# Optimization experiments

Hardware: AMD Instinct MI355X
Metric: run time of the kernel (lower is better)

The kernel has to match this reference:

```python
import jax, jax.numpy as jnp
import numpy as np

PC_RANGE = [-51.2, -51.2, -5.0, 51.2, 51.2, 3.0]
VOXEL = [0.1, 0.1, 0.2]
OSF = 8
NUM_PRIOR = 100
C = 256
BN_EPS = 1e-5
LN_EPS = 1e-5


def _conv(x, w, pad):
    # x: [B,C,H,W], w: [O,I,kh,kw]
    return jax.lax.conv_general_dilated(
        x, w, window_strides=(1, 1), padding=[(pad, pad), (pad, pad)],
        dimension_numbers=('NCHW', 'OIHW', 'NCHW'))


def _bn(x, g, b, m, v):
    scale = (g / jnp.sqrt(v + BN_EPS))[None, :, None, None]
    return (x - m[None, :, None, None]) * scale + b[None, :, None, None]


def setup_inputs() -> dict:
    key = jax.random.key(0)
    ks = jax.random.split(key, 24)
    s3 = 1.0 / np.sqrt(C * 9)
    s1 = 1.0 / np.sqrt(C)
    inp = {
        'bev_feat': jax.random.normal(ks[0], (4, C, 128, 128), jnp.float32),
        'template_anchor': jax.random.normal(ks[1], (4, 900, 11), jnp.float32),
        # shared_conv: 3x3 conv (no bias) + BN(eval) + ReLU
        'shared_w': jax.random.normal(ks[2], (C, C, 3, 3), jnp.float32) * s3,
        'bn1_g': jax.random.normal(ks[3], (C,), jnp.float32) * 0.1 + 1.0,
        'bn1_b': jax.random.normal(ks[4], (C,), jnp.float32) * 0.1,
        'bn1_m': jax.random.normal(ks[5], (C,), jnp.float32) * 0.1,
        'bn1_v': jax.random.uniform(ks[6], (C,), jnp.float32) + 0.5,
        # objectness: 3x3 conv (no bias) + BN + ReLU + 1x1 conv (bias=-2)
        'obj_w1': jax.random.normal(ks[7], (C, C, 3, 3), jnp.float32) * s3,
        'bn2_g': jax.random.normal(ks[8], (C,), jnp.float32) * 0.1 + 1.0,
        'bn2_b': jax.random.normal(ks[9], (C,), jnp.float32) * 0.1,
        'bn2_m': jax.random.normal(ks[10], (C,), jnp.float32) * 0.1,
        'bn2_v': jax.random.uniform(ks[11], (C,), jnp.float32) + 0.5,
        'obj_w2': jax.random.normal(ks[12], (1, C, 1, 1), jnp.float32) * s1,
        'obj_b2': jnp.full((1,), -2.0, jnp.float32),
        # feat_proj: Linear + LN + ReLU + Linear
        'fp_w1': jax.random.normal(ks[13], (C, C), jnp.float32) * s1,
        'fp_b1': jax.random.normal(ks[14], (C,), jnp.float32) * 0.01,
        'ln_g': jnp.ones((C,), jnp.float32),
        'ln_b': jnp.zeros((C,), jnp.float32),
        'fp_w2': jax.random.normal(ks[15], (C, C), jnp.float32) * s1,
        'fp_b2': jax.random.normal(ks[16], (C,), jnp.float32) * 0.01,
        # geometry heads (1x1 convs, bias init 0)
        'z_w': jax.random.normal(ks[17], (1, C, 1, 1), jnp.float32) * s1,
        'z_b': jnp.zeros((1,), jnp.float32),
        'dim_w': jax.random.normal(ks[18], (3, C, 1, 1), jnp.float32) * s1,
        'dim_b': jnp.zeros((3,), jnp.float32),
        'yaw_w': jax.random.normal(ks[19], (2, C, 1, 1), jnp.float32) * s1,
        'yaw_b': jnp.zeros((2,), jnp.float32),
        'vel_w': jax.random.normal(ks[20], (2, C, 1, 1), jnp.float32) * s1,
        'vel_b': jnp.zeros((2,), jnp.float32),
    }
    return inp


def _forward(bev_feat, template_anchor, shared_w, bn1_g, bn1_b, bn1_m, bn1_v,
             obj_w1, bn2_g, bn2_b, bn2_m, bn2_v, obj_w2, obj_b2,
             fp_w1, fp_b1, ln_g, ln_b, fp_w2, fp_b2,
             z_w, z_b, dim_w, dim_b, yaw_w, yaw_b, vel_w, vel_b):
    B, Cc, H, W = bev_feat.shape
    # shared_conv
    feat = jax.nn.relu(_bn(_conv(bev_feat, shared_w, 1), bn1_g, bn1_b, bn1_m, bn1_v))
    # objectness heatmap
    h = jax.nn.relu(_bn(_conv(feat, obj_w1, 1), bn2_g, bn2_b, bn2_m, bn2_v))
    heatmap = jax.nn.sigmoid(_conv(h, obj_w2, 0) + obj_b2[None, :, None, None])
    score = heatmap.reshape(B, H * W)
    K = min(NUM_PRIOR, H * W, template_anchor.shape[1])
    topk_score, topk_inds = jax.lax.top_k(score, K)  # [B,K]
    ys = topk_inds // W
    xs = topk_inds % W
    # gather BEV features at topk locations: [B,K,C]
    feat_flat = feat.reshape(B, Cc, H * W).transpose(0, 2, 1)
    gathered = jnp.take_along_axis(feat_flat, topk_inds[:, :, None], axis=1)
    # feat_proj: Linear + LN + ReLU + Linear
    x = gathered @ fp_w1.T + fp_b1
    mu = jnp.mean(x, axis=-1, keepdims=True)
    var = jnp.mean((x - mu) ** 2, axis=-1, keepdims=True)
    x = (x - mu) / jnp.sqrt(var + LN_EPS) * ln_g + ln_b
    x = jax.nn.relu(x)
    prior_feature = x @ fp_w2.T + fp_b2
    prior_feature = prior_feature * (1.0 + topk_score[:, :, None])
    # geometry heads (1x1 convs == linear on gathered features)
    z_pred = gathered @ z_w[:, :, 0, 0].T + z_b      # [B,K,1]
    dim_pred = gathered @ dim_w[:, :, 0, 0].T + dim_b  # [B,K,3]
    yaw_pred = gathered @ yaw_w[:, :, 0, 0].T + yaw_b  # [B,K,2]
    vel_pred = gathered @ vel_w[:, :, 0, 0].T + vel_b  # [B,K,2]
    # anchor update
    pa = template_anchor[:, :K, :]
    x_metric = (xs.astype(pa.dtype) + 0.5) * (VOXEL[0] * OSF) + PC_RANGE[0]
    y_metric = (ys.astype(pa.dtype) + 0.5) * (VOXEL[1] * OSF) + PC_RANGE[1]
    z_new = pa[..., 2] + 0.5 * z_pred[..., 0]
    dims_new = pa[..., 3:6] + 0.2 * jnp.clip(dim_pred, -1.0, 1.0)
    yaw = jnp.tanh(yaw_pred)
    nrm = jnp.maximum(jnp.sqrt(jnp.sum(yaw * yaw, axis=-1, keepdims=True)), 1e-6)
    yaw_new = 0.7 * pa[..., 6:8] + 0.3 * (yaw / nrm)
    vel_new = pa[..., 8:10] + 0.2 * jnp.clip(vel_pred, -2.0, 2.0)
    prior_anchor = jnp.concatenate([
        x_metric[..., None], y_metric[..., None], z_new[..., None],
        dims_new, yaw_new, vel_new, pa[..., 10:]], axis=-1)
    return prior_feature, prior_anchor, topk_score


def reference(bev_feat, template_anchor, shared_w, bn1_g, bn1_b, bn1_m, bn1_v,
              obj_w1, bn2_g, bn2_b, bn2_m, bn2_v, obj_w2, obj_b2,
              fp_w1, fp_b1, ln_g, ln_b, fp_w2, fp_b2,
              z_w, z_b, dim_w, dim_b, yaw_w, yaw_b, vel_w, vel_b):
    return _forward(bev_feat, template_anchor, shared_w, bn1_g, bn1_b, bn1_m, bn1_v,
                    obj_w1, bn2_g, bn2_b, bn2_m, bn2_v, obj_w2, obj_b2,
                    fp_w1, fp_b1, ln_g, ln_b, fp_w2, fp_b2,
                    z_w, z_b, dim_w, dim_b, yaw_w, yaw_b, vel_w, vel_b)
```

## Files before the change

kernel.cpp:

```cpp
#include <hip/hip_runtime.h>
#include <math.h>


typedef __attribute__((ext_vector_type(8))) short bf16x8;
typedef __attribute__((ext_vector_type(4))) float f32x4;

#define HW 16384
#define WPITCH 130
#define CCAP 192
#define PSTR 28
#define WSO_XN    0ULL
#define WSO_FEATB 34078720ULL
#define WSO_WP1   68157440ULL
#define WSO_WP2   69337088ULL
#define WSO_BNP   70516736ULL
#define WSO_LOG   70521856ULL
#define WSO_CAND  70784000ULL
#define WSO_CNT   70787072ULL
#define WSO_EXL   70787136ULL
#define WSO_TIDX  70790208ULL
#define WSO_TLOG  70791808ULL
#define WSO_W1N   70793408ULL
#define WSO_W2N   73152704ULL
#define WSO_A1P   WSO_XN
#define WSO_ACC2  28311552ULL

__device__ __forceinline__ float bf2f(short s) {
  return __uint_as_float(((unsigned)(unsigned short)s) << 16);
}
__device__ __forceinline__ short f2bf(float f) {
  unsigned u = __float_as_uint(f);
  u += 0x7fffu + ((u >> 16) & 1u);
  return (short)(u >> 16);
}
__device__ __forceinline__ void gll16(const void* g, void* l) {
  __builtin_amdgcn_global_load_lds(
      (const __attribute__((address_space(1))) void*)g,
      (__attribute__((address_space(3))) void*)l, 16, 0, 0);
}

__global__ void wprep2(const float* __restrict__ s1, const float* __restrict__ s2,
                       short* __restrict__ wp1, short* __restrict__ wp2,
                       float* __restrict__ wn1, float* __restrict__ wn2) {
  int bx = blockIdx.x;
  const float* src;
  short* wp;
  float* wn;
  if (bx >= 2304) {
    src = s2; wp = wp2; wn = wn2; bx -= 2304;
  } else {
    src = s1; wp = wp1; wn = wn1;
  }
  int i = bx * 256 + threadIdx.x;
  float v = src[i];
  int k = i % 9;
  int r = i / 9;
  int ci = r & 255;
  int co = r >> 8;
  wp[(k * 256 + co) * 256 + ci] = f2bf(v);
  wn[(ci * 9 + k) * 256 + co] = v;
}

__global__ void smallprep(const float* g1, const float* b1, const float* m1,
                          const float* v1, const float* g2, const float* b2,
                          const float* m2, const float* v2, const float* w2,
                          const float* ob2, float* __restrict__ bnp,
                          short* __restrict__ xn, short* __restrict__ featb,
                          float* __restrict__ logits) {
  const int blk = blockIdx.x, t = threadIdx.x;
  if (blk < 1024) {
    int i = blk * 256 + t;
    int c = i & 255;
    int r = i >> 8;
    int nh = r >> 1;
    int side = r & 1;
    size_t off = ((size_t)nh * WPITCH + (side ? 129 : 0)) * 256 + c;
    xn[off] = 0;
    featb[off] = 0;
  } else if (blk < 1280) {
    logits[(blk - 1024) * 256 + t] = ob2[0];
  } else {
    float s1 = g1[t] / sqrtf(v1[t] + 1e-5f);
    bnp[t] = s1;
    bnp[256 + t] = b1[t] - m1[t] * s1;
    float s2 = g2[t] / sqrtf(v2[t] + 1e-5f);
    bnp[512 + t] = s2;
    bnp[768 + t] = b2[t] - m2[t] * s2;
    bnp[1024 + t] = w2[t];
  }
}

__global__ __launch_bounds__(256) void nchw2nhwc(const float* __restrict__ in,
                                                 short* __restrict__ out) {
  __shared__ short tl[64 * 66];
  int n = blockIdx.z, c0 = blockIdx.y * 64, s0 = blockIdx.x * 64;
  int sl = threadIdx.x & 63, cl = threadIdx.x >> 6;
  for (int p = 0; p < 16; ++p) {
    int c = cl + p * 4;
    tl[c * 66 + sl] = f2bf(in[(((size_t)(n * 256 + c0 + c)) << 14) + s0 + sl]);
  }
  __syncthreads();
  int co = threadIdx.x & 63, so = threadIdx.x >> 6;
  for (int p = 0; p < 16; ++p) {
    int S = s0 + so + p * 4;
    int h = S >> 7, w = S & 127;
    out[(((size_t)(n * 128 + h)) * WPITCH + w + 1) * 256 + c0 + co] =
        tl[co * 66 + (so + p * 4)];
  }
}

template <int OUT_LOGITS>
__global__ __launch_bounds__(256, 2) void conv3x3(const short* __restrict__ inp,
                                                  const short* __restrict__ wp,
                                                  const float* __restrict__ scale,
                                                  const float* __restrict__ shift,
                                                  const float* __restrict__ w2f,
                                                  short* __restrict__ outb,
                                                  float* __restrict__ logits) {
  __shared__ short a_sm[2][132 * 32];
  __shared__ short b_sm[3][128 * 32];
  const int t = threadIdx.x;
  const int wv = t >> 6, lane = t & 63;
  const int l15 = lane & 15, quad = lane >> 4;
  const int tile = blockIdx.x;
  const int img = tile >> 6;
  const int h0 = (tile & 63) << 1;
  const int nblk = blockIdx.y;
  const int m0 = (wv & 1) << 6;
  const int n0 = (wv >> 1) << 6;

  f32x4 acc[2][4][4];
#pragma unroll
  for (int r = 0; r < 2; ++r)
#pragma unroll
    for (int i = 0; i < 4; ++i)
#pragma unroll
      for (int j = 0; j < 4; ++j) {
        acc[r][i][j][0] = 0.f; acc[r][i][j][1] = 0.f;
        acc[r][i][j][2] = 0.f; acc[r][i][j][3] = 0.f;
      }

  for (int dhi = 0; dhi < 3; ++dhi) {
    const int hy0 = h0 + dhi - 1;
    const int hy1 = hy0 + 1;
    const bool v0 = (hy0 >= 0) && (hy0 <= 127);
    const bool v1 = (hy1 <= 127);
    const size_t arow0 = ((size_t)(img * 128 + hy0)) * WPITCH;
    const size_t arow1 = ((size_t)(img * 128 + hy1)) * WPITCH;
    const short* wbase = wp + ((size_t)(dhi * 3 * 256 + nblk * 128)) * 256;

    for (int c0 = 0; c0 < 256; c0 += 32) {
      __syncthreads();
      if (v0) {
#pragma unroll
        for (int j = 0; j < 2; ++j) {
          const int seg = (j << 6) + (t >> 2);
          const int cc = t & 3;
          gll16(inp + (arow0 + seg) * 256 + c0 + cc * 8,
                a_sm[0] + ((size_t)((j << 8) + t)) * 8);
        }
      }
      if (v1) {
#pragma unroll
        for (int j = 0; j < 2; ++j) {
          const int seg = (j << 6) + (t >> 2);
          const int cc = t & 3;
          gll16(inp + (arow1 + seg) * 256 + c0 + cc * 8,
                a_sm[1] + ((size_t)((j << 8) + t)) * 8);
        }
      }
      if (t < 64) {
        const int row = t >> 5;
        const bool vr = row ? v1 : v0;
        if (vr) {
          const size_t ar = row ? arow1 : arow0;
          const int rem = t & 31;
          const int r2 = rem >> 4, dw = rem & 15;
          const int* gsrc = (const int*)(inp + (ar + 128 + r2) * 256 + c0) + dw;
          ((int*)a_sm[row])[(128 + r2) * 16 + dw] = *gsrc;
        }
      }
#pragma unroll
      for (int dwi = 0; dwi < 3; ++dwi) {
        const short* wtap = wbase + (size_t)dwi * 65536;
#pragma unroll
        for (int j = 0; j < 2; ++j) {
          const int nrow = (j << 6) + (t >> 2);
          const int cc = t & 3;
          gll16(wtap + (size_t)nrow * 256 + c0 + cc * 8,
                b_sm[dwi] + ((size_t)((j << 8) + t)) * 8);
        }
      }
      __syncthreads();

#pragma unroll
      for (int dwi = 0; dwi < 3; ++dwi) {
        bf16x8 bfr[4];
#pragma unroll
        for (int i = 0; i < 4; ++i)
          bfr[i] = *(const bf16x8*)(b_sm[dwi] + (n0 + i * 16 + l15) * 32 + quad * 8);
        if (v0) {
          bf16x8 af[4];
#pragma unroll
          for (int i = 0; i < 4; ++i)
            af[i] = *(const bf16x8*)(a_sm[0] + (dwi + m0 + i * 16 + l15) * 32 + quad * 8);
#pragma unroll
          for (int i = 0; i < 4; ++i)
#pragma unroll
            for (int j = 0; j < 4; ++j)
              acc[0][i][j] = __builtin_amdgcn_mfma_f32_16x16x32_bf16(
                  af[i], bfr[j], acc[0][i][j], 0, 0, 0);
        }
        if (v1) {
          bf16x8 af[4];
#pragma unroll
          for (int i = 0; i < 4; ++i)
            af[i] = *(const bf16x8*)(a_sm[1] + (dwi + m0 + i * 16 + l15) * 32 + quad * 8);
#pragma unroll
          for (int i = 0; i < 4; ++i)
#pragma unroll
            for (int j = 0; j < 4; ++j)
              acc[1][i][j] = __builtin_amdgcn_mfma_f32_16x16x32_bf16(
                  af[i], bfr[j], acc[1][i][j], 0, 0, 0);
        }
      }
    }
  }

  float sc[4], sh[4], wf[4];
#pragma unroll
  for (int j = 0; j < 4; ++j) {
    const int co = nblk * 128 + n0 + j * 16 + l15;
    sc[j] = scale[co];
    sh[j] = shift[co];
    if (OUT_LOGITS) wf[j] = w2f[co];
  }
#pragma unroll
  for (int r = 0; r < 2; ++r) {
    if (OUT_LOGITS) {
      float* lrow = logits + ((size_t)img << 14) + ((h0 + r) << 7);
#pragma unroll
      for (int i = 0; i < 4; ++i) {
#pragma unroll
        for (int rg = 0; rg < 4; ++rg) {
          float part = 0.f;
#pragma unroll
          for (int j = 0; j < 4; ++j) {
            float v = fmaxf(acc[r][i][j][rg] * sc[j] + sh[j], 0.f);
            part += v * wf[j];
          }
          part += __shfl_xor(part, 1);
          part += __shfl_xor(part, 2);
          part += __shfl_xor(part, 4);
          part += __shfl_xor(part, 8);
          if (l15 == 0)
            atomicAdd(&lrow[m0 + i * 16 + quad * 4 + rg], part);
        }
      }
    } else {
      const size_t obase = ((size_t)(img * 128 + h0 + r)) * WPITCH + 1;
#pragma unroll
      for (int i = 0; i < 4; ++i) {
#pragma unroll
        for (int j = 0; j < 4; ++j) {
          const int co = nblk * 128 + n0 + j * 16 + l15;
#pragma unroll
          for (int rg = 0; rg < 4; ++rg) {
            const int m = m0 + i * 16 + quad * 4 + rg;
            float v = fmaxf(acc[r][i][j][rg] * sc[j] + sh[j], 0.f);
            outb[(obase + m) * 256 + co] = f2bf(v);
          }
        }
      }
    }
  }
}

__global__ __launch_bounds__(1024) void topk_radix(const float* __restrict__ logits,
                                                   int* __restrict__ cand,
                                                   int* __restrict__ cnt_out) {
  __shared__ int hist[2048];
  __shared__ int wsum[16];
  __shared__ unsigned sel_bin;
  __shared__ int sel_above;
  __shared__ int cntr;
  const int b = blockIdx.x, t = threadIdx.x;
  const int lane = t & 63, wid = t >> 6;
  const float* L = logits + (size_t)b * HW;
  const int base = t * 16;
  unsigned kv[16];
#pragma unroll
  for (int i = 0; i < 4; ++i) {
    float4 v = *(const float4*)(L + base + i * 4);
    float f4[4] = {v.x, v.y, v.z, v.w};
#pragma unroll
    for (int j = 0; j < 4; ++j) {
      unsigned u = __float_as_uint(f4[j]);
      kv[i * 4 + j] = u ^ (((unsigned)((int)u >> 31)) | 0x80000000u);
    }
  }
  unsigned prefix = 0, pmask = 0;
  int need = 128;
  const int shifts[3] = {21, 10, 0};
  const int nbs[3] = {2048, 2048, 1024};

  for (int lev = 0; lev < 3; ++lev) {
    const int shift = shifts[lev];
    const int nb = nbs[lev];
    hist[t] = 0;
    hist[t + 1024] = 0;
    __syncthreads();
#pragma unroll
    for (int i = 0; i < 16; ++i)
      if ((kv[i] & pmask) == prefix)
        atomicAdd(&hist[(kv[i] >> shift) & (nb - 1)], 1);
    __syncthreads();
    const int cs = nb >> 10;
    const int bin_hi = nb - 1 - t * cs;
    const int c_hi = hist[bin_hi];
    const int c_lo = (cs == 2) ? hist[bin_hi - 1] : 0;
    const int s = c_hi + c_lo;
    int inc = s;
    for (int off = 1; off < 64; off <<= 1) {
      int nbr = __shfl_up(inc, off);
      if (lane >= off) inc += nbr;
    }
    if (lane == 63) wsum[wid] = inc;
    __syncthreads();
    if (wid == 0) {
      int wv = (lane < 16) ? wsum[lane] : 0;
      for (int off = 1; off < 16; off <<= 1) {
        int nbr = __shfl_up(wv, off);
        if (lane >= off) wv += nbr;
      }
      if (lane < 16) wsum[lane] = wv;
    }
    __syncthreads();
    const int excl = inc - s + (wid ? wsum[wid - 1] : 0);
    if (excl < need && need <= excl + s) {
      if (need <= excl + c_hi) {
        sel_bin = (unsigned)bin_hi;
        sel_above = excl;
      } else {
        sel_bin = (unsigned)(bin_hi - 1);
        sel_above = excl + c_hi;
      }
    }
    __syncthreads();
    prefix |= sel_bin << shift;
    pmask |= ((unsigned)(nb - 1)) << shift;
    need -= sel_above;
    __syncthreads();
  }
  if (t == 0) cntr = 0;
  __syncthreads();
#pragma unroll
  for (int i = 0; i < 16; ++i) {
    if (kv[i] >= prefix) {
      int p = atomicAdd(&cntr, 1);
      if (p < CCAP) cand[b * CCAP + p] = base + i;
    }
  }
  __syncthreads();
  if (t == 0) cnt_out[b] = (cntr < CCAP) ? cntr : CCAP;
}

__device__ __forceinline__ void wload4(const float* __restrict__ wr,
                                       float w[4][9]) {
#pragma unroll
  for (int k = 0; k < 9; ++k)
#pragma unroll
    for (int h = 0; h < 4; ++h)
      w[h][k] = wr[k * 256 + (h << 6)];
}

__device__ __forceinline__ void conv_step(const float* __restrict__ pc,
                                          const float w[4][9], float a[4][9]) {
  float xp[28];
  const float4* pr = (const float4*)pc;
#pragma unroll
  for (int q = 0; q < 7; ++q) {
    float4 v = pr[q];
    xp[q * 4 + 0] = v.x; xp[q * 4 + 1] = v.y;
    xp[q * 4 + 2] = v.z; xp[q * 4 + 3] = v.w;
  }
#pragma unroll
  for (int py = 0; py < 3; ++py)
#pragma unroll
    for (int px = 0; px < 3; ++px)
#pragma unroll
      for (int ky = 0; ky < 3; ++ky)
#pragma unroll
        for (int kx = 0; kx < 3; ++kx) {
          const float xv = xp[(py + ky) * 5 + px + kx];
          const int pp = py * 3 + px, kk = ky * 3 + kx;
          a[0][pp] += w[0][kk] * xv;
          a[1][pp] += w[1][kk] * xv;
          a[2][pp] += w[2][kk] * xv;
          a[3][pp] += w[3][kk] * xv;
        }
}

__global__ __launch_bounds__(256, 2) void rescore_a(
    const float* __restrict__ bev, const float* __restrict__ w1n,
    const int* __restrict__ cand, const int* __restrict__ cnt,
    float* __restrict__ a1part) {
  const int bx = blockIdx.x, b = blockIdx.y, z = blockIdx.z;
  const int t = threadIdx.x;
  const int n = cnt[b];
  const int c0 = bx * 4;
  if (c0 >= n) return;
  const int nc = (n - c0 < 4) ? (n - c0) : 4;
  const int ci0 = z << 6;
  __shared__ float patch[4 * 64 * PSTR];

  {
    const int TE = nc * 1600;
    int sg[4];
#pragma unroll
    for (int g = 0; g < 4; ++g) {
      int cc = c0 + g;
      sg[g] = cand[b * CCAP + ((cc < n) ? cc : (n - 1))];
    }
#pragma unroll
    for (int k = 0; k < 25; ++k) {
      int e = t + (k << 8);
      if (e < TE) {
        int g = (e >= 3200) ? ((e >= 4800) ? 3 : 2) : ((e >= 1600) ? 1 : 0);
        int rem = e - g * 1600;
        int ci = rem / 25;
        int rj = rem - ci * 25;
        int r = rj / 5;
        int j = rj - r * 5;
        int s = sg[g];
        int hy = (s >> 7) - 2 + r, wx = (s & 127) - 2 + j;
        float v = 0.f;
        if (hy >= 0 && hy < 128 && wx >= 0 && wx < 128)
          v = bev[(((size_t)(b * 256 + ci0 + ci)) << 14) + (hy << 7) + wx];
        patch[(g * 64 + ci) * PSTR + rj] = v;
      } else {
        int g2z = (e >= 3200) ? ((e >= 4800) ? 3 : 2) : 1;
        int rem = e - g2z * 1600;
        int ci = rem / 25;
        int rj = rem - ci * 25;
        patch[(g2z * 64 + ci) * PSTR + rj] = 0.f;
      }
    }
  }
  __syncthreads();

  const int col = t & 63;
  const int g = t >> 6;
  float a[4][9];
#pragma unroll
  for (int h = 0; h < 4; ++h)
#pragma unroll
    for (int p = 0; p < 9; ++p) a[h][p] = 0.f;

  const float* pbase = patch + (g << 6) * PSTR;
  const float* wbase = w1n + (size_t)ci0 * 2304 + col;

  float wA[4][9], wB[4][9];
  wload4(wbase, wA);
  for (int ci = 0; ci < 64; ci += 2) {
    wload4(wbase + (size_t)(ci + 1) * 2304, wB);
    conv_step(pbase + ci * PSTR, wA, a);
    if (ci + 2 < 64)
      wload4(wbase + (size_t)(ci + 2) * 2304, wA);
    conv_step(pbase + (ci + 1) * PSTR, wB, a);
  }

  if (g < nc) {
    const int c = c0 + g;
    float* dst =
        a1part + ((((size_t)(b * CCAP + c) * 4 + z) * 9) << 8) + col;
#pragma unroll
    for (int p = 0; p < 9; ++p)
#pragma unroll
      for (int h = 0; h < 4; ++h)
        dst[(p << 8) + (h << 6)] = a[h][p];
  }
}

__global__ __launch_bounds__(256) void rescore_b(const float* __restrict__ a1part,
                                                 const float* __restrict__ w2n,
                                                 const float* __restrict__ bnp,
                                                 const int* __restrict__ cnt,
                                                 float* __restrict__ acc2) {
  const int bx = blockIdx.x, b = blockIdx.y, z = blockIdx.z;
  const int t = threadIdx.x;
  const int n = cnt[b];
  const int cbase = bx * 8;
  if (cbase >= n) return;
  const int zb = z << 6;
  __shared__ float f9[8 * 64 * 12];

  const int cf = t & 63;
  const int pg = t >> 6;
  const int cfg = zb + cf;
  const float sc1 = bnp[cfg], sh1 = bnp[256 + cfg];
#pragma unroll
  for (int g = 0; g < 8; ++g) {
    const int c = cbase + g;
    if (c < n) {
      const float* src =
          a1part + ((((size_t)(b * CCAP + c)) * 36) << 8) + cfg;
      for (int p = pg; p < 9; p += 4) {
        float v = src[(size_t)(0 * 9 + p) << 8] + src[(size_t)(1 * 9 + p) << 8] +
                  src[(size_t)(2 * 9 + p) << 8] + src[(size_t)(3 * 9 + p) << 8];
        f9[(g * 64 + cf) * 12 + p] = fmaxf(v * sc1 + sh1, 0.f);
      }
    } else {
      for (int p = pg; p < 9; p += 4) f9[(g * 64 + cf) * 12 + p] = 0.f;
    }
  }
  __syncthreads();

  float acc[8];
#pragma unroll
  for (int g = 0; g < 8; ++g) acc[g] = 0.f;
  for (int ci = 0; ci < 64; ++ci) {
    const float* wr = w2n + (size_t)(zb + ci) * 2304 + t;
    float w9[9];
#pragma unroll
    for (int k = 0; k < 9; ++k) w9[k] = wr[k * 256];
#pragma unroll
    for (int g = 0; g < 8; ++g) {
      const float4* fp = (const float4*)(f9 + (g * 64 + ci) * 12);
      float4 f0 = fp[0], f1 = fp[1], f2 = fp[2];
      acc[g] += w9[0] * f0.x;
      acc[g] += w9[1] * f0.y;
      acc[g] += w9[2] * f0.z;
      acc[g] += w9[3] * f0.w;
      acc[g] += w9[4] * f1.x;
      acc[g] += w9[5] * f1.y;
      acc[g] += w9[6] * f1.z;
      acc[g] += w9[7] * f1.w;
      acc[g] += w9[8] * f2.x;
    }
  }
#pragma unroll
  for (int g = 0; g < 8; ++g) {
    const int c = cbase + g;
    if (c < n)
      acc2[((((size_t)(b * CCAP + c)) * 4 + z) << 8) + t] = acc[g];
  }
}

__global__ __launch_bounds__(256) void rescore_c(const float* __restrict__ acc2,
                                                 const float* __restrict__ bnp,
                                                 const float* __restrict__ b2,
                                                 const int* __restrict__ cnt,
                                                 float* __restrict__ exlog) {
  const int bx = blockIdx.x, b = blockIdx.y, t = threadIdx.x;
  const int lane = t & 63, wid = t >> 6;
  const int n = cnt[b];
  const int c = bx * 4 + wid;
  if (c >= n) return;
  const float* src = acc2 + (((size_t)(b * CCAP + c)) << 10);
  float p = 0.f;
#pragma unroll
  for (int j = 0; j < 4; ++j) {
    const int co = lane + j * 64;
    float v = ((src[co] + src[256 + co]) + src[512 + co]) + src[768 + co];
    p += fmaxf(v * bnp[512 + co] + bnp[768 + co], 0.f) * bnp[1024 + co];
  }
  for (int off = 32; off; off >>= 1) p += __shfl_xor(p, off);
  if (lane == 0) exlog[b * CCAP + c] = p + b2[0];
}

__global__ __launch_bounds__(CCAP) void final_topk(const float* __restrict__ exlog,
                                                   const int* __restrict__ cand,
                                                   const int* __restrict__ cnt,
                                                   int* __restrict__ tidx,
                                                   float* __restrict__ tlog) {
  const int b = blockIdx.x, t = threadIdx.x;
  __shared__ float v[CCAP];
  __shared__ int si[CCAP];
  const int n = cnt[b];
  float mv = (t < n) ? exlog[b * CCAP + t] : -3.0e38f;
  int s = (t < n) ? cand[b * CCAP + t] : 0x7FFFFFFF;
  v[t] = mv;
  si[t] = s;
  __syncthreads();
  int rank = 0;
  for (int j = 0; j < CCAP; ++j) {
    float vj = v[j];
    int sj = si[j];
    if (vj > mv || (vj == mv && sj < s)) ++rank;
  }
  if (t < n && rank < 100) {
    tidx[b * 100 + rank] = s;
    tlog[b * 100 + rank] = mv;
  }
}

__global__ __launch_bounds__(256) void head_kern(
    const short* __restrict__ featb, const int* __restrict__ tidx,
    const float* __restrict__ tlog, const float* __restrict__ tmpl,
    const float* __restrict__ w1, const float* __restrict__ b1,
    const float* __restrict__ lng, const float* __restrict__ lnb,
    const float* __restrict__ w2, const float* __restrict__ b2,
    const float* __restrict__ zw, const float* __restrict__ zb,
    const float* __restrict__ dmw, const float* __restrict__ dmb,
    const float* __restrict__ yw, const float* __restrict__ yb,
    const float* __restrict__ vw, const float* __restrict__ vb,
    float* __restrict__ out) {
  const int blk = blockIdx.x;
  const int b = blk / 100, q = blk % 100;
  const int t = threadIdx.x;
  const int lane = t & 63, wid = t >> 6;
  __shared__ float g[256];
  __shared__ float sx[256];
  __shared__ float red[4];
  __shared__ float heads[8];

  const int s = tidx[b * 100 + q];
  const float score = 1.f / (1.f + expf(-tlog[b * 100 + q]));
  const int ys = s >> 7, xs = s & 127;

  g[t] = bf2f(featb[(((size_t)(b * 128 + ys)) * WPITCH + xs + 1) * 256 + t]);
  __syncthreads();

  float x = b1[t];
  {
    const float* wr = w1 + (size_t)t * 256;
    for (int i = 0; i < 256; i += 4) {
      float4 wv = *(const float4*)(wr + i);
      x += g[i] * wv.x + g[i + 1] * wv.y + g[i + 2] * wv.z + g[i + 3] * wv.w;
    }
  }
  float sum = x;
  for (int off = 32; off; off >>= 1) sum += __shfl_xor(sum, off);
  if (lane == 0) red[wid] = sum;
  __syncthreads();
  float mu = (red[0] + red[1] + red[2] + red[3]) * (1.f / 256.f);
  __syncthreads();
  float d = x - mu;
  float q2 = d * d;
  for (int off = 32; off; off >>= 1) q2 += __shfl_xor(q2, off);
  if (lane == 0) red[wid] = q2;
  __syncthreads();
  float var = (red[0] + red[1] + red[2] + red[3]) * (1.f / 256.f);
  float xn = d * (1.f / sqrtf(var + 1e-5f)) * lng[t] + lnb[t];
  xn = fmaxf(xn, 0.f);
  sx[t] = xn;
  __syncthreads();
  float pf = b2[t];
  {
    const float* wr = w2 + (size_t)t * 256;
    for (int i = 0; i < 256; i += 4) {
      float4 wv = *(const float4*)(wr + i);
      pf += sx[i] * wv.x + sx[i + 1] * wv.y + sx[i + 2] * wv.z + sx[i + 3] * wv.w;
    }
  }
  pf *= (1.f + score);
  out[(size_t)(b * 100 + q) * 256 + t] = pf;

  const int k = t >> 5, l = t & 31;
  const float* hw;
  float hb;
  if (k == 0)      { hw = zw;                 hb = zb[0]; }
  else if (k < 4)  { hw = dmw + (k - 1) * 256; hb = dmb[k - 1]; }
  else if (k < 6)  { hw = yw + (k - 4) * 256;  hb = yb[k - 4]; }
  else             { hw = vw + (k - 6) * 256;  hb = vb[k - 6]; }
  float hp = 0.f;
#pragma unroll
  for (int r = 0; r < 8; ++r) {
    int i = l + r * 32;
    hp += g[i] * hw[i];
  }
  for (int off = 16; off; off >>= 1) hp += __shfl_xor(hp, off);
  if (l == 0) heads[k] = hp + hb;
  __syncthreads();

  if (t == 0) {
    const float* pa = tmpl + ((size_t)b * 900 + q) * 11;
    float p[11];
#pragma unroll
    for (int i = 0; i < 11; ++i) p[i] = pa[i];
    float a[11];
    a[0] = ((float)xs + 0.5f) * 0.8f - 51.2f;
    a[1] = ((float)ys + 0.5f) * 0.8f - 51.2f;
    a[2] = p[2] + 0.5f * heads[0];
#pragma unroll
    for (int i = 0; i < 3; ++i)
      a[3 + i] = p[3 + i] + 0.2f * fminf(fmaxf(heads[1 + i], -1.f), 1.f);
    float t0 = tanhf(heads[4]), t1 = tanhf(heads[5]);
    float nrm = fmaxf(sqrtf(t0 * t0 + t1 * t1), 1e-6f);
    a[6] = 0.7f * p[6] + 0.3f * t0 / nrm;
    a[7] = 0.7f * p[7] + 0.3f * t1 / nrm;
    a[8] = p[8] + 0.2f * fminf(fmaxf(heads[6], -2.f), 2.f);
    a[9] = p[9] + 0.2f * fminf(fmaxf(heads[7], -2.f), 2.f);
    a[10] = p[10];
    float* oa = out + 102400 + (size_t)(b * 100 + q) * 11;
#pragma unroll
    for (int i = 0; i < 11; ++i) oa[i] = a[i];
    out[106800 + b * 100 + q] = score;
  }
}

extern "C" void kernel_launch(void* const* d_in, const int* in_sizes, int n_in,
                              void* d_out, int out_size, void* d_ws, size_t ws_size,
                              hipStream_t stream) {
  (void)in_sizes; (void)n_in; (void)out_size; (void)ws_size;
  char* ws = (char*)d_ws;
  short* xn     = (short*)(ws + WSO_XN);
  short* featb  = (short*)(ws + WSO_FEATB);
  short* wp1    = (short*)(ws + WSO_WP1);
  short* wp2    = (short*)(ws + WSO_WP2);
  float* bnp    = (float*)(ws + WSO_BNP);
  float* logits = (float*)(ws + WSO_LOG);
  int*   cand   = (int*)(ws + WSO_CAND);
  int*   cnt    = (int*)(ws + WSO_CNT);
  float* exl    = (float*)(ws + WSO_EXL);
  int*   tidx   = (int*)(ws + WSO_TIDX);
  float* tlog   = (float*)(ws + WSO_TLOG);
  float* w1n    = (float*)(ws + WSO_W1N);
  float* w2n    = (float*)(ws + WSO_W2N);
  float* a1p    = (float*)(ws + WSO_A1P);
  float* acc2   = (float*)(ws + WSO_ACC2);

  const float* bev = (const float*)d_in[0];

  wprep2<<<4608, 256, 0, stream>>>((const float*)d_in[2], (const float*)d_in[7],
                                   wp1, wp2, w1n, w2n);
  smallprep<<<1281, 256, 0, stream>>>(
      (const float*)d_in[3], (const float*)d_in[4], (const float*)d_in[5],
      (const float*)d_in[6], (const float*)d_in[8], (const float*)d_in[9],
      (const float*)d_in[10], (const float*)d_in[11], (const float*)d_in[12],
      (const float*)d_in[13], bnp, xn, featb, logits);
  nchw2nhwc<<<dim3(256, 4, 4), 256, 0, stream>>>(bev, xn);
  conv3x3<0><<<dim3(256, 2), 256, 0, stream>>>(xn, wp1, bnp, bnp + 256,
                                               nullptr, featb, nullptr);
  conv3x3<1><<<dim3(256, 2), 256, 0, stream>>>(featb, wp2, bnp + 512, bnp + 768,
                                               bnp + 1024, nullptr, logits);
  topk_radix<<<4, 1024, 0, stream>>>(logits, cand, cnt);
  rescore_a<<<dim3(CCAP / 4, 4, 4), 256, 0, stream>>>(bev, w1n, cand, cnt, a1p);
  rescore_b<<<dim3(CCAP / 8, 4, 4), 256, 0, stream>>>(a1p, w2n, bnp, cnt, acc2);
  rescore_c<<<dim3(CCAP / 4, 4), 256, 0, stream>>>(acc2, bnp,
                                                   (const float*)d_in[13], cnt,
                                                   exl);
  final_topk<<<4, CCAP, 0, stream>>>(exl, cand, cnt, tidx, tlog);
  head_kern<<<400, 256, 0, stream>>>(
      featb, tidx, tlog, (const float*)d_in[1],
      (const float*)d_in[14], (const float*)d_in[15], (const float*)d_in[16],
      (const float*)d_in[17], (const float*)d_in[18], (const float*)d_in[19],
      (const float*)d_in[20], (const float*)d_in[21], (const float*)d_in[22],
      (const float*)d_in[23], (const float*)d_in[24], (const float*)d_in[25],
      (const float*)d_in[26], (const float*)d_in[27], (float*)d_out);
}
```

Before: 494.7 us.

## Share weight loads across two candidates per wave in rescore_a with split-K reduction

In rescore_a, each wave now computes two candidates over half of the 64 input channels, instead of one candidate over all 64. Each weight load is therefore reused for two patches, which halves per-thread weight traffic from global memory. The two channel halves are then combined through a shared-memory reduction. In exchange, each thread holds twice as many accumulators, which adds register pressure, and the reduction adds extra syncs and LDS traffic.

After: 569.6 us. +15.2%, slower.

```diff
diff --git a/kernel.cpp b/kernel.cpp
--- a/kernel.cpp
+++ b/kernel.cpp
@@ -412,7 +412,8 @@
   if (c0 >= n) return;
   const int nc = (n - c0 < 4) ? (n - c0) : 4;
   const int ci0 = z << 6;
-  __shared__ float patch[4 * 64 * PSTR];
+  __shared__ float shbuf[9472];
+  float* patch = shbuf;
 
   {
     const int TE = nc * 1600;
@@ -450,35 +451,61 @@
   __syncthreads();
 
   const int col = t & 63;
-  const int g = t >> 6;
-  float a[4][9];
+  const int w = t >> 6;
+  const int p = w & 1;
+  const int cih = w >> 1;
+  float aA[4][9], aB[4][9];
 #pragma unroll
   for (int h = 0; h < 4; ++h)
 #pragma unroll
-    for (int p = 0; p < 9; ++p) a[h][p] = 0.f;
-
-  const float* pbase = patch + (g << 6) * PSTR;
-  const float* wbase = w1n + (size_t)ci0 * 2304 + col;
+    for (int q = 0; q < 9; ++q) { aA[h][q] = 0.f; aB[h][q] = 0.f; }
+
+  const float* pA = patch + ((p * 2 + 0) * 64 + cih * 32) * PSTR;
+  const float* pB = patch + ((p * 2 + 1) * 64 + cih * 32) * PSTR;
+  const float* wbase = w1n + (size_t)(ci0 + cih * 32) * 2304 + col;
 
   float wA[4][9], wB[4][9];
   wload4(wbase, wA);
-  for (int ci = 0; ci < 64; ci += 2) {
+  for (int ci = 0; ci < 32; ci += 2) {
     wload4(wbase + (size_t)(ci + 1) * 2304, wB);
-    conv_step(pbase + ci * PSTR, wA, a);
-    if (ci + 2 < 64)
+    conv_step(pA + ci * PSTR, wA, aA);
+    conv_step(pB + ci * PSTR, wA, aB);
+    if (ci + 2 < 32)
       wload4(wbase + (size_t)(ci + 2) * 2304, wA);
-    conv_step(pbase + (ci + 1) * PSTR, wB, a);
-  }
-
-  if (g < nc) {
-    const int c = c0 + g;
-    float* dst =
-        a1part + ((((size_t)(b * CCAP + c) * 4 + z) * 9) << 8) + col;
-#pragma unroll
-    for (int p = 0; p < 9; ++p)
+    conv_step(pA + (ci + 1) * PSTR, wB, aA);
+    conv_step(pB + (ci + 1) * PSTR, wB, aB);
+  }
+
+  __syncthreads();
+  float* comb = shbuf;
+  if (cih == 0) {
+#pragma unroll
+    for (int gg = 0; gg < 2; ++gg) {
+      float* cb = comb + (((p * 2 + gg) * 64) + col) * 37;
+      const float (*a)[9] = gg ? aB : aA;
 #pragma unroll
       for (int h = 0; h < 4; ++h)
-        dst[(p << 8) + (h << 6)] = a[h][p];
+#pragma unroll
+        for (int q = 0; q < 9; ++q) cb[h * 9 + q] = a[h][q];
+    }
+  }
+  __syncthreads();
+  if (cih == 1) {
+#pragma unroll
+    for (int gg = 0; gg < 2; ++gg) {
+      const int c = c0 + p * 2 + gg;
+      if (c < n) {
+        const float* cb = comb + (((p * 2 + gg) * 64) + col) * 37;
+        float (*a)[9] = gg ? aB : aA;
+        float* dst =
+            a1part + ((((size_t)(b * CCAP + c) * 4 + z) * 9) << 8) + col;
+#pragma unroll
+        for (int q = 0; q < 9; ++q)
+#pragma unroll
+          for (int h = 0; h < 4; ++h)
+            dst[(q << 8) + (h << 6)] = cb[h * 9 + q] + a[h][q];
+      }
+    }
   }
 }
 
```
